# Optimization experiments

Hardware: AMD Instinct MI355X
Metric: run time of the kernel (lower is better)

Reference implementation:

```python
import jax, jax.numpy as jnp
import numpy as np

N = 40000   # nodes
E = 640000  # edges (no self loops; module adds them)
IN = 64     # in_channels
H = 8       # heads
C = 16      # hidden_channels (per head)
ED = 3      # edge_dim
OUT = 32    # last_layer_output
NEG_SLOPE = 0.2  # GATv2Conv default negative_slope


def setup_inputs() -> dict:
    key = jax.random.key(0)
    ks = jax.random.split(key, 16)
    x = jax.random.normal(ks[0], (N, IN), jnp.float32)
    src = jax.random.randint(ks[1], (E,), 0, N)
    off = jax.random.randint(ks[2], (E,), 1, N)
    dst = (src + off) % N  # guarantees no pre-existing self loops (PyG removes them anyway)
    edge_attr = jax.random.normal(ks[3], (E, ED), jnp.float32)
    HC = H * C

    def lin(k, o, i):
        return jax.random.normal(k, (o, i), jnp.float32) * (1.0 / np.sqrt(i))

    params = dict(
        Wl1=lin(ks[4], HC, IN), bl1=jnp.zeros((HC,), jnp.float32),
        Wr1=lin(ks[5], HC, IN), br1=jnp.zeros((HC,), jnp.float32),
        We1=lin(ks[6], HC, ED),
        att1=jax.random.normal(ks[7], (H, C), jnp.float32) * 0.1,
        b1=jnp.zeros((HC,), jnp.float32),
        Wl2=lin(ks[8], HC, HC), bl2=jnp.zeros((HC,), jnp.float32),
        Wr2=lin(ks[9], HC, HC), br2=jnp.zeros((HC,), jnp.float32),
        We2=lin(ks[10], HC, ED),
        att2=jax.random.normal(ks[11], (H, C), jnp.float32) * 0.1,
        b2=jnp.zeros((HC,), jnp.float32),
        Wf=lin(ks[12], OUT, HC), bf=jnp.zeros((OUT,), jnp.float32),
    )
    return {"x": x, "edge_src": src, "edge_dst": dst, "edge_attr": edge_attr, **params}


def _add_self_loops(src, dst, eattr):
    # PyG add_self_loops with fill_value='mean': self-loop attr = mean of incoming edge attrs
    sums = jax.ops.segment_sum(eattr, dst, num_segments=N)
    cnt = jax.ops.segment_sum(jnp.ones((eattr.shape[0], 1), eattr.dtype), dst, num_segments=N)
    loop = jnp.where(cnt > 0, sums / jnp.maximum(cnt, 1.0), 0.0)
    ar = jnp.arange(N)
    return (jnp.concatenate([src, ar]), jnp.concatenate([dst, ar]),
            jnp.concatenate([eattr, loop], axis=0))


def _gatv2(x, src, dst, eattr, Wl, bl, Wr, br, We, att, bias):
    xl = (x @ Wl.T + bl).reshape(-1, H, C)  # source-side transform
    xr = (x @ Wr.T + br).reshape(-1, H, C)  # target-side transform
    e = (eattr @ We.T).reshape(-1, H, C)    # edge embedding (no bias in PyG)
    m = jax.nn.leaky_relu(xl[src] + xr[dst] + e, NEG_SLOPE)  # [E', H, C]
    alpha = jnp.einsum('ehc,hc->eh', m, att)                 # attention logits
    amax = jax.ops.segment_max(alpha, dst, num_segments=N)
    ex = jnp.exp(alpha - amax[dst])
    denom = jax.ops.segment_sum(ex, dst, num_segments=N)
    a = ex / (denom[dst] + 1e-16)                            # PyG softmax epsilon
    out = jax.ops.segment_sum(xl[src] * a[:, :, None], dst, num_segments=N)
    return out.reshape(-1, H * C) + bias                      # concat heads + layer bias


def reference(x, edge_src, edge_dst, edge_attr,
              Wl1, bl1, Wr1, br1, We1, att1, b1,
              Wl2, bl2, Wr2, br2, We2, att2, b2,
              Wf, bf):
    src, dst, ea = _add_self_loops(edge_src, edge_dst, edge_attr)
    h = jax.nn.elu(_gatv2(x, src, dst, ea, Wl1, bl1, Wr1, br1, We1, att1, b1))
    h = jax.nn.elu(_gatv2(h, src, dst, ea, Wl2, bl2, Wr2, br2, We2, att2, b2))
    return h @ Wf.T + bf
```

## Files before the change

### kernel.cpp

```cpp
#include <hip/hip_runtime.h>
#include <hip/hip_fp16.h>
#include <math.h>

#define NNODES 40000
#define NEDGES 640000
#define NETOT  (NEDGES + NNODES)
#define HC 128
#define OUTC 32
#define NBLK   ((NNODES + 255) / 256)

typedef __attribute__((ext_vector_type(8))) _Float16 v8h;
typedef __attribute__((ext_vector_type(2))) _Float16 v2h;
typedef __attribute__((ext_vector_type(4))) float    v4f;

__device__ __forceinline__ unsigned splat_h(float f)
{
    unsigned short h = __half_as_ushort(__float2half(f));
    return ((unsigned)h << 16) | h;
}
__device__ __forceinline__ float h_lo(unsigned u)
{
    return __half2float(__ushort_as_half((unsigned short)(u & 0xffff)));
}
__device__ __forceinline__ v2h h2bits(unsigned u)
{
    union { unsigned u; v2h h; } c; c.u = u; return c.h;
}

#define CB ((NEDGES + 255) / 256)
#define SX4 (NNODES * 64 / 4)
#define CONV (SX4 + 2 * 128 * 64 + 2 * 128 * 128)

__global__ void count_convert_kernel(const int* __restrict__ dst, int* __restrict__ cnt,
                                     int* __restrict__ slot,
                                     const float* __restrict__ x,
                                     const float* __restrict__ Wl1, const float* __restrict__ Wr1,
                                     const float* __restrict__ Wl2, const float* __restrict__ Wr2,
                                     __half* __restrict__ x16,
                                     __half* __restrict__ WH1, __half* __restrict__ WH2)
{
    int b = blockIdx.x;
    if (b < CB) {
        int e = b * 256 + threadIdx.x;
        if (e >= NEDGES) return;
        slot[e] = atomicAdd(&cnt[dst[e]], 1);
        return;
    }
    int i = (b - CB) * 256 + threadIdx.x;
    if (i < SX4) {
        float4 v = ((const float4*)x)[i];
        __half tmp[4] = {__float2half(v.x), __float2half(v.y),
                         __float2half(v.z), __float2half(v.w)};
        ((uint2*)x16)[i] = *(const uint2*)tmp;
        return;
    }
    int j = i - SX4;
    if (j < 128 * 64)            { WH1[j] = __float2half(Wl1[j]); return; }
    j -= 128 * 64;
    if (j < 128 * 64)            { WH1[128 * 64 + j] = __float2half(Wr1[j]); return; }
    j -= 128 * 64;
    if (j < 128 * 128)           { WH2[j] = __float2half(Wl2[j]); return; }
    j -= 128 * 128;
    if (j < 128 * 128)           { WH2[128 * 128 + j] = __float2half(Wr2[j]); return; }
}

__global__ __launch_bounds__(256) void scan1_kernel(const int* __restrict__ cnt,
                                                    int* __restrict__ offsets,
                                                    int* __restrict__ blocksum)
{
    __shared__ int s[256];
    int t = threadIdx.x;
    int n = blockIdx.x * 256 + t;
    int v = (n < NNODES) ? (cnt[n] + 1) : 0;
    s[t] = v;
    __syncthreads();
    for (int off = 1; off < 256; off <<= 1) {
        int u = (t >= off) ? s[t - off] : 0;
        __syncthreads();
        s[t] += u;
        __syncthreads();
    }
    if (n < NNODES) offsets[n] = s[t] - v;
    if (t == 255) blocksum[blockIdx.x] = s[255];
}

__global__ __launch_bounds__(256) void scan2_kernel(int* __restrict__ blocksum)
{
    __shared__ int s[256];
    int t = threadIdx.x;
    int v = (t < NBLK) ? blocksum[t] : 0;
    s[t] = v;
    __syncthreads();
    for (int off = 1; off < 256; off <<= 1) {
        int u = (t >= off) ? s[t - off] : 0;
        __syncthreads();
        s[t] += u;
        __syncthreads();
    }
    if (t < NBLK) blocksum[t] = s[t] - v;
}

__global__ __launch_bounds__(256) void scan3_kernel(int* __restrict__ offsets,
                                                    const int* __restrict__ blocksum)
{
    int n = blockIdx.x * 256 + threadIdx.x;
    if (n >= NNODES) return;
    offsets[n] += blocksum[blockIdx.x];
    if (n == 0) offsets[NNODES] = NETOT;
}

__global__ void place_kernel(const int* __restrict__ src, const int* __restrict__ dst,
                             const float* __restrict__ eattr,
                             const int* __restrict__ offsets, const int* __restrict__ slot,
                             uint4* __restrict__ csr4)
{
    int e = blockIdx.x * blockDim.x + threadIdx.x;
    if (e >= NEDGES) return;
    int d = dst[e];
    int pos = offsets[d] + slot[e];
    uint4 rec;
    rec.x = (unsigned)src[e];
    rec.y = splat_h(eattr[e * 3 + 0]);
    rec.z = splat_h(eattr[e * 3 + 1]);
    rec.w = splat_h(eattr[e * 3 + 2]);
    csr4[pos] = rec;
}

__global__ __launch_bounds__(256) void loopattr_kernel(const int* __restrict__ offsets,
                                                       uint4* __restrict__ csr4)
{
    int n = blockIdx.x * 256 + threadIdx.x;
    if (n >= NNODES) return;
    int beg = offsets[n], endr = offsets[n + 1] - 1;
    float s0 = 0.f, s1 = 0.f, s2 = 0.f;
    for (int j = beg; j < endr; j++) {
        uint4 q = csr4[j];
        s0 += h_lo(q.y); s1 += h_lo(q.z); s2 += h_lo(q.w);
    }
    int c = endr - beg;
    float inv = (c > 0) ? (1.0f / (float)c) : 0.0f;
    uint4 rec;
    rec.x = (unsigned)n;
    rec.y = splat_h(s0 * inv);
    rec.z = splat_h(s1 * inv);
    rec.w = splat_h(s2 * inv);
    csr4[endr] = rec;
}

template <int K>
__global__ __launch_bounds__(256) void transform_mfma_kernel(
    const __half* __restrict__ X16, const __half* __restrict__ WH,
    const float* __restrict__ bl, const float* __restrict__ br,
    __half* __restrict__ XLo, __half* __restrict__ XRo)
{
    int t = threadIdx.x;
    int w = t >> 6, lane = t & 63;
    int nb = blockIdx.x * 32;
    int mb = w * 64;
    int l15 = lane & 15, lg = lane >> 4;

    v4f acc[4][2];
#pragma unroll
    for (int mt = 0; mt < 4; mt++)
#pragma unroll
        for (int nt = 0; nt < 2; nt++) acc[mt][nt] = (v4f){0.f, 0.f, 0.f, 0.f};

#pragma unroll
    for (int kb = 0; kb < K; kb += 32) {
        int kf = kb + lg * 8;
        v8h bfr[2], afr[4];
#pragma unroll
        for (int nt = 0; nt < 2; nt++)
            bfr[nt] = *(const v8h*)&X16[(size_t)(nb + nt * 16 + l15) * K + kf];
#pragma unroll
        for (int mt = 0; mt < 4; mt++)
            afr[mt] = *(const v8h*)&WH[(size_t)(mb + mt * 16 + l15) * K + kf];
#pragma unroll
        for (int mt = 0; mt < 4; mt++)
#pragma unroll
            for (int nt = 0; nt < 2; nt++)
                acc[mt][nt] = __builtin_amdgcn_mfma_f32_16x16x32_f16(
                    afr[mt], bfr[nt], acc[mt][nt], 0, 0, 0);
    }

    bool isR = mb >= 128;
    const float* bias = isR ? br : bl;
    __half* Out       = isR ? XRo : XLo;
    int cb = (mb & 127);
#pragma unroll
    for (int mt = 0; mt < 4; mt++) {
        int cc = cb + mt * 16 + lg * 4;
        float b0 = bias[cc], b1 = bias[cc + 1], b2 = bias[cc + 2], b3 = bias[cc + 3];
#pragma unroll
        for (int nt = 0; nt < 2; nt++) {
            int n = nb + nt * 16 + l15;
            __half tmp[4] = {__float2half(acc[mt][nt][0] + b0),
                             __float2half(acc[mt][nt][1] + b1),
                             __float2half(acc[mt][nt][2] + b2),
                             __float2half(acc[mt][nt][3] + b3)};
            *(uint2*)&Out[(size_t)n * HC + cc] = *(const uint2*)tmp;
        }
    }
}

template <int CTRL>
__device__ __forceinline__ float dpp_swap(float x)
{
    return __int_as_float(__builtin_amdgcn_update_dpp(
        0, __float_as_int(x), CTRL, 0xF, 0xF, true));
}

template <int FUSE>
__global__ __launch_bounds__(256) void agg_kernel(
    const __half* __restrict__ XL, const __half* __restrict__ XR,
    const uint4* __restrict__ csr4, const int* __restrict__ offsets,
    const float* __restrict__ We, const float* __restrict__ att,
    const float* __restrict__ bias, __half* __restrict__ OUT,
    const float* __restrict__ Wf, const float* __restrict__ bf,
    float* __restrict__ out2)
{
    __shared__ float wf_s[FUSE ? OUTC * 132 : 1];
    __shared__ float hrow[FUSE ? 4 * HC : 1];

    int t = threadIdx.x;
    if (FUSE) {
        for (int i = t * 4; i < OUTC * HC; i += 1024) {
            float4 v = *(const float4*)&Wf[i];
            *(float4*)&wf_s[(i >> 7) * 132 + (i & 127)] = v;
        }
        __syncthreads();
    }

    int w = t >> 6;
    int n = __builtin_amdgcn_readfirstlane(blockIdx.x * 4 + w);
    int lane = t & 63;
    int c0 = lane * 2;

    const float LOG2E = 1.44269504088896340736f;
    v2h xr2 = *(const v2h*)&XR[(size_t)n * HC + c0];
    float2 atf = *(const float2*)&att[c0];
    v2h at2 = {(_Float16)(atf.x * LOG2E), (_Float16)(atf.y * LOG2E)};
    v2h we0 = {(_Float16)We[c0 * 3 + 0], (_Float16)We[c0 * 3 + 3]};
    v2h we1 = {(_Float16)We[c0 * 3 + 1], (_Float16)We[c0 * 3 + 4]};
    v2h we2 = {(_Float16)We[c0 * 3 + 2], (_Float16)We[c0 * 3 + 5]};
    const v2h vk02 = {(_Float16)0.2f, (_Float16)0.2f};

    int beg = offsets[n], end = offsets[n + 1];

    float dacc[8], a0[8], a1[8];
#pragma unroll
    for (int i = 0; i < 8; i++) { dacc[i] = 0.f; a0[i] = 0.f; a1[i] = 0.f; }

#define EDGE_STEP(q, xl2, d_, a0_, a1_)                                        \
    {                                                                          \
        v2h m2 = xl2 + xr2;                                                    \
        m2 += we0 * h2bits(q.y);                                               \
        m2 += we1 * h2bits(q.z);                                               \
        m2 += we2 * h2bits(q.w);                                               \
        v2h lk = m2 * vk02;                                                    \
        m2 = __builtin_elementwise_max(m2, lk);                                \
        float p;                                                               \
        p = __builtin_amdgcn_fdot2(m2, at2, 0.0f, false);                      \
        p += dpp_swap<0xB1>(p);                                                \
        p += dpp_swap<0x4E>(p);                                                \
        p += dpp_swap<0x141>(p);                                               \
        float ex = exp2f(p);                                                   \
        d_  += ex;                                                             \
        a0_ = fmaf(ex, (float)xl2.x, a0_);                                     \
        a1_ = fmaf(ex, (float)xl2.y, a1_);                                     \
    }

    int j = beg;
    for (; j + 7 < end; j += 8) {
        uint4 q[8];
        v2h   xl[8];
#pragma unroll
        for (int i = 0; i < 8; i++) q[i] = csr4[j + i];
#pragma unroll
        for (int i = 0; i < 8; i++) {
            int s = __builtin_amdgcn_readfirstlane((int)q[i].x);
            xl[i] = *(const v2h*)&XL[((size_t)s << 7) + c0];
        }
#pragma unroll
        for (int i = 0; i < 8; i++)
            EDGE_STEP(q[i], xl[i], dacc[i], a0[i], a1[i]);
    }
    if (j + 3 < end) {
        uint4 q[4];
        v2h   xl[4];
#pragma unroll
        for (int i = 0; i < 4; i++) q[i] = csr4[j + i];
#pragma unroll
        for (int i = 0; i < 4; i++) {
            int s = __builtin_amdgcn_readfirstlane((int)q[i].x);
            xl[i] = *(const v2h*)&XL[((size_t)s << 7) + c0];
        }
#pragma unroll
        for (int i = 0; i < 4; i++)
            EDGE_STEP(q[i], xl[i], dacc[i], a0[i], a1[i]);
        j += 4;
    }
    for (; j < end; j++) {
        uint4 q = csr4[j];
        int s = __builtin_amdgcn_readfirstlane((int)q.x);
        v2h xl = *(const v2h*)&XL[((size_t)s << 7) + c0];
        EDGE_STEP(q, xl, dacc[0], a0[0], a1[0]);
    }
#undef EDGE_STEP

    float den  = ((dacc[0] + dacc[1]) + (dacc[2] + dacc[3])) +
                 ((dacc[4] + dacc[5]) + (dacc[6] + dacc[7]));
    float acc0 = ((a0[0] + a0[1]) + (a0[2] + a0[3])) +
                 ((a0[4] + a0[5]) + (a0[6] + a0[7]));
    float acc1 = ((a1[0] + a1[1]) + (a1[2] + a1[3])) +
                 ((a1[4] + a1[5]) + (a1[6] + a1[7]));

    float inv = 1.0f / (den + 1e-16f);
    float o0 = acc0 * inv + bias[c0];
    float o1 = acc1 * inv + bias[c0 + 1];
    o0 = (o0 > 0.f) ? o0 : expm1f(o0);
    o1 = (o1 > 0.f) ? o1 : expm1f(o1);

    if (!FUSE) {
        __half2 hv = __floats2half2_rn(o0, o1);
        *(__half2*)&OUT[(size_t)n * HC + c0] = hv;
    } else {
        hrow[w * HC + c0]     = o0;
        hrow[w * HC + c0 + 1] = o1;
        int o = lane & 31, half = lane >> 5;
        const float* hr = &hrow[w * HC + half * 64];
        const float* wr = &wf_s[o * 132 + half * 64];
        float acc = 0.f;
#pragma unroll
        for (int c = 0; c < 64; c += 4) {
            float4 hv = *(const float4*)&hr[c];
            float4 wv = *(const float4*)&wr[c];
            acc = fmaf(hv.x, wv.x, acc);
            acc = fmaf(hv.y, wv.y, acc);
            acc = fmaf(hv.z, wv.z, acc);
            acc = fmaf(hv.w, wv.w, acc);
        }
        acc += __shfl_xor(acc, 32);
        if (lane < 32) out2[(size_t)n * OUTC + o] = acc + bf[o];
    }
}

extern "C" void kernel_launch(void* const* d_in, const int* in_sizes, int n_in,
                              void* d_out, int out_size, void* d_ws, size_t ws_size,
                              hipStream_t stream)
{
    const float* x     = (const float*)d_in[0];
    const int*   esrc  = (const int*)d_in[1];
    const int*   edst  = (const int*)d_in[2];
    const float* eattr = (const float*)d_in[3];
    const float* Wl1 = (const float*)d_in[4];  const float* bl1 = (const float*)d_in[5];
    const float* Wr1 = (const float*)d_in[6];  const float* br1 = (const float*)d_in[7];
    const float* We1 = (const float*)d_in[8];  const float* att1 = (const float*)d_in[9];
    const float* b1  = (const float*)d_in[10];
    const float* Wl2 = (const float*)d_in[11]; const float* bl2 = (const float*)d_in[12];
    const float* Wr2 = (const float*)d_in[13]; const float* br2 = (const float*)d_in[14];
    const float* We2 = (const float*)d_in[15]; const float* att2 = (const float*)d_in[16];
    const float* b2  = (const float*)d_in[17];
    const float* Wf  = (const float*)d_in[18]; const float* bf  = (const float*)d_in[19];

    char* ws = (char*)d_ws;
    size_t off = 0;
    auto alloc = [&](size_t bytes) -> void* {
        void* p = ws + off;
        off += (bytes + 255) & ~(size_t)255;
        return p;
    };
    int*    cnt      = (int*)alloc((size_t)NNODES * 4);
    int*    offsets  = (int*)alloc((size_t)(NNODES + 1) * 4);
    int*    slot     = (int*)alloc((size_t)NEDGES * 4);
    uint4*  csr4     = (uint4*)alloc((size_t)NETOT * 16);
    int*    blocksum = (int*)alloc((size_t)NBLK * 4);
    __half* x16      = (__half*)alloc((size_t)NNODES * 64 * 2);
    __half* WH1      = (__half*)alloc((size_t)256 * 64 * 2);
    __half* WH2      = (__half*)alloc((size_t)256 * 128 * 2);
    __half* XL       = (__half*)alloc((size_t)NNODES * HC * 2);
    __half* XR       = (__half*)alloc((size_t)NNODES * HC * 2);
    __half* H1       = (__half*)alloc((size_t)NNODES * HC * 2);

    hipMemsetAsync(cnt, 0, (size_t)NNODES * 4, stream);

    count_convert_kernel<<<CB + (CONV + 255) / 256, 256, 0, stream>>>(
        edst, cnt, slot, x, Wl1, Wr1, Wl2, Wr2, x16, WH1, WH2);
    scan1_kernel<<<NBLK, 256, 0, stream>>>(cnt, offsets, blocksum);
    scan2_kernel<<<1, 256, 0, stream>>>(blocksum);
    scan3_kernel<<<NBLK, 256, 0, stream>>>(offsets, blocksum);
    place_kernel<<<(NEDGES + 255) / 256, 256, 0, stream>>>(esrc, edst, eattr, offsets, slot, csr4);
    loopattr_kernel<<<NBLK, 256, 0, stream>>>(offsets, csr4);

    transform_mfma_kernel<64><<<NNODES / 32, 256, 0, stream>>>(x16, WH1, bl1, br1, XL, XR);
    agg_kernel<0><<<NNODES / 4, 256, 0, stream>>>(XL, XR, csr4, offsets,
                                                  We1, att1, b1, H1, nullptr, nullptr, nullptr);
    transform_mfma_kernel<128><<<NNODES / 32, 256, 0, stream>>>(H1, WH2, bl2, br2, XL, XR);
    agg_kernel<1><<<NNODES / 4, 256, 0, stream>>>(XL, XR, csr4, offsets,
                                                  We2, att2, b2, nullptr, Wf, bf, (float*)d_out);
}
```

Measured before the change: 189.3 us.

## Pack CSR edge records into 8 bytes and fuse placement with first transform

Edge records shrink from 16 to 8 bytes by packing a 16-bit source index with three half-precision edge attributes. The aggregation kernels re-splat the attributes after a scalar readfirstlane. This halves CSR traffic in placement, self-loop averaging and both aggregation passes. The edge placement kernel and the layer-1 MFMA transform now run as one launch with split block ranges, removing a launch and letting the two overlap. The 16-bit source index limits node count to 65536.

```diff
diff --git a/kernel.cpp b/kernel.cpp
--- a/kernel.cpp
+++ b/kernel.cpp
@@ -13,18 +13,17 @@
 typedef __attribute__((ext_vector_type(2))) _Float16 v2h;
 typedef __attribute__((ext_vector_type(4))) float    v4f;
 
-__device__ __forceinline__ unsigned splat_h(float f)
-{
-    unsigned short h = __half_as_ushort(__float2half(f));
-    return ((unsigned)h << 16) | h;
-}
-__device__ __forceinline__ float h_lo(unsigned u)
-{
-    return __half2float(__ushort_as_half((unsigned short)(u & 0xffff)));
-}
 __device__ __forceinline__ v2h h2bits(unsigned u)
 {
     union { unsigned u; v2h h; } c; c.u = u; return c.h;
+}
+__device__ __forceinline__ float h_at(unsigned u, int hi)
+{
+    return __half2float(__ushort_as_half((unsigned short)(hi ? (u >> 16) : (u & 0xffff))));
+}
+__device__ __forceinline__ unsigned hbits(float f)
+{
+    return (unsigned)__half_as_ushort(__float2half(f));
 }
 
 #define CB ((NEDGES + 255) / 256)
@@ -109,53 +108,15 @@
     if (n == 0) offsets[NNODES] = NETOT;
 }
 
-__global__ void place_kernel(const int* __restrict__ src, const int* __restrict__ dst,
-                             const float* __restrict__ eattr,
-                             const int* __restrict__ offsets, const int* __restrict__ slot,
-                             uint4* __restrict__ csr4)
-{
-    int e = blockIdx.x * blockDim.x + threadIdx.x;
-    if (e >= NEDGES) return;
-    int d = dst[e];
-    int pos = offsets[d] + slot[e];
-    uint4 rec;
-    rec.x = (unsigned)src[e];
-    rec.y = splat_h(eattr[e * 3 + 0]);
-    rec.z = splat_h(eattr[e * 3 + 1]);
-    rec.w = splat_h(eattr[e * 3 + 2]);
-    csr4[pos] = rec;
-}
-
-__global__ __launch_bounds__(256) void loopattr_kernel(const int* __restrict__ offsets,
-                                                       uint4* __restrict__ csr4)
-{
-    int n = blockIdx.x * 256 + threadIdx.x;
-    if (n >= NNODES) return;
-    int beg = offsets[n], endr = offsets[n + 1] - 1;
-    float s0 = 0.f, s1 = 0.f, s2 = 0.f;
-    for (int j = beg; j < endr; j++) {
-        uint4 q = csr4[j];
-        s0 += h_lo(q.y); s1 += h_lo(q.z); s2 += h_lo(q.w);
-    }
-    int c = endr - beg;
-    float inv = (c > 0) ? (1.0f / (float)c) : 0.0f;
-    uint4 rec;
-    rec.x = (unsigned)n;
-    rec.y = splat_h(s0 * inv);
-    rec.z = splat_h(s1 * inv);
-    rec.w = splat_h(s2 * inv);
-    csr4[endr] = rec;
-}
-
 template <int K>
-__global__ __launch_bounds__(256) void transform_mfma_kernel(
+__device__ __forceinline__ void transform_body(
+    int bx, int t,
     const __half* __restrict__ X16, const __half* __restrict__ WH,
     const float* __restrict__ bl, const float* __restrict__ br,
     __half* __restrict__ XLo, __half* __restrict__ XRo)
 {
-    int t = threadIdx.x;
     int w = t >> 6, lane = t & 63;
-    int nb = blockIdx.x * 32;
+    int nb = bx * 32;
     int mb = w * 64;
     int l15 = lane & 15, lg = lane >> 4;
 
@@ -203,6 +164,58 @@
     }
 }
 
+template <int K>
+__global__ __launch_bounds__(256) void transform_mfma_kernel(
+    const __half* __restrict__ X16, const __half* __restrict__ WH,
+    const float* __restrict__ bl, const float* __restrict__ br,
+    __half* __restrict__ XLo, __half* __restrict__ XRo)
+{
+    transform_body<K>(blockIdx.x, threadIdx.x, X16, WH, bl, br, XLo, XRo);
+}
+
+__global__ __launch_bounds__(256) void place_transform_kernel(
+    const int* __restrict__ src, const int* __restrict__ dst,
+    const float* __restrict__ eattr,
+    const int* __restrict__ offsets, const int* __restrict__ slot,
+    uint2* __restrict__ csr2,
+    const __half* __restrict__ X16, const __half* __restrict__ WH,
+    const float* __restrict__ bl, const float* __restrict__ br,
+    __half* __restrict__ XLo, __half* __restrict__ XRo)
+{
+    int b = blockIdx.x;
+    if (b < CB) {
+        int e = b * 256 + threadIdx.x;
+        if (e >= NEDGES) return;
+        int d = dst[e];
+        int pos = offsets[d] + slot[e];
+        uint2 rec;
+        rec.x = (unsigned)src[e] | (hbits(eattr[e * 3 + 0]) << 16);
+        rec.y = hbits(eattr[e * 3 + 1]) | (hbits(eattr[e * 3 + 2]) << 16);
+        csr2[pos] = rec;
+        return;
+    }
+    transform_body<64>(b - CB, threadIdx.x, X16, WH, bl, br, XLo, XRo);
+}
+
+__global__ __launch_bounds__(256) void loopattr_kernel(const int* __restrict__ offsets,
+                                                       uint2* __restrict__ csr2)
+{
+    int n = blockIdx.x * 256 + threadIdx.x;
+    if (n >= NNODES) return;
+    int beg = offsets[n], endr = offsets[n + 1] - 1;
+    float s0 = 0.f, s1 = 0.f, s2 = 0.f;
+    for (int j = beg; j < endr; j++) {
+        uint2 q = csr2[j];
+        s0 += h_at(q.x, 1); s1 += h_at(q.y, 0); s2 += h_at(q.y, 1);
+    }
+    int c = endr - beg;
+    float inv = (c > 0) ? (1.0f / (float)c) : 0.0f;
+    uint2 rec;
+    rec.x = (unsigned)n | (hbits(s0 * inv) << 16);
+    rec.y = hbits(s1 * inv) | (hbits(s2 * inv) << 16);
+    csr2[endr] = rec;
+}
+
 template <int CTRL>
 __device__ __forceinline__ float dpp_swap(float x)
 {
@@ -213,7 +226,7 @@
 template <int FUSE>
 __global__ __launch_bounds__(256) void agg_kernel(
     const __half* __restrict__ XL, const __half* __restrict__ XR,
-    const uint4* __restrict__ csr4, const int* __restrict__ offsets,
+    const uint2* __restrict__ csr2, const int* __restrict__ offsets,
     const float* __restrict__ We, const float* __restrict__ att,
     const float* __restrict__ bias, __half* __restrict__ OUT,
     const float* __restrict__ Wf, const float* __restrict__ bf,
@@ -251,12 +264,22 @@
 #pragma unroll
     for (int i = 0; i < 8; i++) { dacc[i] = 0.f; a0[i] = 0.f; a1[i] = 0.f; }
 
-#define EDGE_STEP(q, xl2, d_, a0_, a1_)                                        \
+#define DECODE(q, s_, e00_, e11_, e22_)                                        \
+    {                                                                          \
+        unsigned qx = (unsigned)__builtin_amdgcn_readfirstlane((int)q.x);      \
+        unsigned qy = (unsigned)__builtin_amdgcn_readfirstlane((int)q.y);      \
+        s_   = (int)(qx & 0xffffu);                                            \
+        e00_ = (qx >> 16) * 0x10001u;                                          \
+        e11_ = (qy & 0xffffu) * 0x10001u;                                      \
+        e22_ = (qy & 0xffff0000u) | (qy >> 16);                                \
+    }
+
+#define EDGE_STEP(e00, e11, e22, xl2, d_, a0_, a1_)                            \
     {                                                                          \
         v2h m2 = xl2 + xr2;                                                    \
-        m2 += we0 * h2bits(q.y);                                               \
-        m2 += we1 * h2bits(q.z);                                               \
-        m2 += we2 * h2bits(q.w);                                               \
+        m2 += we0 * h2bits(e00);                                               \
+        m2 += we1 * h2bits(e11);                                               \
+        m2 += we2 * h2bits(e22);                                               \
         v2h lk = m2 * vk02;                                                    \
         m2 = __builtin_elementwise_max(m2, lk);                                \
         float p;                                                               \
@@ -272,41 +295,47 @@
 
     int j = beg;
     for (; j + 7 < end; j += 8) {
-        uint4 q[8];
+        uint2 q[8];
         v2h   xl[8];
-#pragma unroll
-        for (int i = 0; i < 8; i++) q[i] = csr4[j + i];
+        int      s[8];
+        unsigned e00[8], e11[8], e22[8];
+#pragma unroll
+        for (int i = 0; i < 8; i++) q[i] = csr2[j + i];
 #pragma unroll
         for (int i = 0; i < 8; i++) {
-            int s = __builtin_amdgcn_readfirstlane((int)q[i].x);
-            xl[i] = *(const v2h*)&XL[((size_t)s << 7) + c0];
+            DECODE(q[i], s[i], e00[i], e11[i], e22[i]);
+            xl[i] = *(const v2h*)&XL[((size_t)s[i] << 7) + c0];
         }
 #pragma unroll
         for (int i = 0; i < 8; i++)
-            EDGE_STEP(q[i], xl[i], dacc[i], a0[i], a1[i]);
+            EDGE_STEP(e00[i], e11[i], e22[i], xl[i], dacc[i], a0[i], a1[i]);
     }
     if (j + 3 < end) {
-        uint4 q[4];
+        uint2 q[4];
         v2h   xl[4];
-#pragma unroll
-        for (int i = 0; i < 4; i++) q[i] = csr4[j + i];
+        int      s[4];
+        unsigned e00[4], e11[4], e22[4];
+#pragma unroll
+        for (int i = 0; i < 4; i++) q[i] = csr2[j + i];
 #pragma unroll
         for (int i = 0; i < 4; i++) {
-            int s = __builtin_amdgcn_readfirstlane((int)q[i].x);
-            xl[i] = *(const v2h*)&XL[((size_t)s << 7) + c0];
+            DECODE(q[i], s[i], e00[i], e11[i], e22[i]);
+            xl[i] = *(const v2h*)&XL[((size_t)s[i] << 7) + c0];
         }
 #pragma unroll
         for (int i = 0; i < 4; i++)
-            EDGE_STEP(q[i], xl[i], dacc[i], a0[i], a1[i]);
+            EDGE_STEP(e00[i], e11[i], e22[i], xl[i], dacc[i], a0[i], a1[i]);
         j += 4;
     }
     for (; j < end; j++) {
-        uint4 q = csr4[j];
-        int s = __builtin_amdgcn_readfirstlane((int)q.x);
+        uint2 q = csr2[j];
+        int s; unsigned e00, e11, e22;
+        DECODE(q, s, e00, e11, e22);
         v2h xl = *(const v2h*)&XL[((size_t)s << 7) + c0];
-        EDGE_STEP(q, xl, dacc[0], a0[0], a1[0]);
+        EDGE_STEP(e00, e11, e22, xl, dacc[0], a0[0], a1[0]);
     }
 #undef EDGE_STEP
+#undef DECODE
 
     float den  = ((dacc[0] + dacc[1]) + (dacc[2] + dacc[3])) +
                  ((dacc[4] + dacc[5]) + (dacc[6] + dacc[7]));
@@ -373,7 +402,7 @@
     int*    cnt      = (int*)alloc((size_t)NNODES * 4);
     int*    offsets  = (int*)alloc((size_t)(NNODES + 1) * 4);
     int*    slot     = (int*)alloc((size_t)NEDGES * 4);
-    uint4*  csr4     = (uint4*)alloc((size_t)NETOT * 16);
+    uint2*  csr2     = (uint2*)alloc((size_t)NETOT * 8);
     int*    blocksum = (int*)alloc((size_t)NBLK * 4);
     __half* x16      = (__half*)alloc((size_t)NNODES * 64 * 2);
     __half* WH1      = (__half*)alloc((size_t)256 * 64 * 2);
@@ -389,13 +418,15 @@
     scan1_kernel<<<NBLK, 256, 0, stream>>>(cnt, offsets, blocksum);
     scan2_kernel<<<1, 256, 0, stream>>>(blocksum);
     scan3_kernel<<<NBLK, 256, 0, stream>>>(offsets, blocksum);
-    place_kernel<<<(NEDGES + 255) / 256, 256, 0, stream>>>(esrc, edst, eattr, offsets, slot, csr4);
-    loopattr_kernel<<<NBLK, 256, 0, stream>>>(offsets, csr4);
-
-    transform_mfma_kernel<64><<<NNODES / 32, 256, 0, stream>>>(x16, WH1, bl1, br1, XL, XR);
-    agg_kernel<0><<<NNODES / 4, 256, 0, stream>>>(XL, XR, csr4, offsets,
+
+    place_transform_kernel<<<CB + NNODES / 32, 256, 0, stream>>>(
+        esrc, edst, eattr, offsets, slot, csr2,
+        x16, WH1, bl1, br1, XL, XR);
+    loopattr_kernel<<<NBLK, 256, 0, stream>>>(offsets, csr2);
+
+    agg_kernel<0><<<NNODES / 4, 256, 0, stream>>>(XL, XR, csr2, offsets,
                                                   We1, att1, b1, H1, nullptr, nullptr, nullptr);
     transform_mfma_kernel<128><<<NNODES / 32, 256, 0, stream>>>(H1, WH2, bl2, br2, XL, XR);
-    agg_kernel<1><<<NNODES / 4, 256, 0, stream>>>(XL, XR, csr4, offsets,
+    agg_kernel<1><<<NNODES / 4, 256, 0, stream>>>(XL, XR, csr2, offsets,
                                                   We2, att2, b2, nullptr, Wf, bf, (float*)d_out);
 }
```

Result: faster. 180.2 us (-4.8%).

## Process two edges per wavefront in aggregation and fuse placement with layer-1 transform

Applied to the files above, without the earlier changes.

The aggregation kernel now splits each wavefront into two halves that handle alternating edges, each lane covering 4 channels of a 64-lane half-row instead of 2 channels of a full row. Partial sums are combined across the halves with a shuffle, which halves the per-edge loop trip count and widens the XL gathers. Separately, the CSR placement kernel and the layer-1 MFMA transform are merged into one launch, saving a kernel boundary. In exchange the source index is no longer wave-uniform (readfirstlane is dropped), an odd tail edge needs masking, and the head reduction now spans only two DPP steps within a 4-lane group.

```diff
diff --git a/kernel.cpp b/kernel.cpp
--- a/kernel.cpp
+++ b/kernel.cpp
@@ -13,18 +13,18 @@
 typedef __attribute__((ext_vector_type(2))) _Float16 v2h;
 typedef __attribute__((ext_vector_type(4))) float    v4f;
 
+__device__ __forceinline__ v2h h2bits(unsigned u)
+{
+    union { unsigned u; v2h h; } c; c.u = u; return c.h;
+}
+__device__ __forceinline__ float h_lo(unsigned u)
+{
+    return __half2float(__ushort_as_half((unsigned short)(u & 0xffff)));
+}
 __device__ __forceinline__ unsigned splat_h(float f)
 {
     unsigned short h = __half_as_ushort(__float2half(f));
     return ((unsigned)h << 16) | h;
-}
-__device__ __forceinline__ float h_lo(unsigned u)
-{
-    return __half2float(__ushort_as_half((unsigned short)(u & 0xffff)));
-}
-__device__ __forceinline__ v2h h2bits(unsigned u)
-{
-    union { unsigned u; v2h h; } c; c.u = u; return c.h;
 }
 
 #define CB ((NEDGES + 255) / 256)
@@ -109,21 +109,95 @@
     if (n == 0) offsets[NNODES] = NETOT;
 }
 
-__global__ void place_kernel(const int* __restrict__ src, const int* __restrict__ dst,
-                             const float* __restrict__ eattr,
-                             const int* __restrict__ offsets, const int* __restrict__ slot,
-                             uint4* __restrict__ csr4)
-{
-    int e = blockIdx.x * blockDim.x + threadIdx.x;
-    if (e >= NEDGES) return;
-    int d = dst[e];
-    int pos = offsets[d] + slot[e];
-    uint4 rec;
-    rec.x = (unsigned)src[e];
-    rec.y = splat_h(eattr[e * 3 + 0]);
-    rec.z = splat_h(eattr[e * 3 + 1]);
-    rec.w = splat_h(eattr[e * 3 + 2]);
-    csr4[pos] = rec;
+template <int K>
+__device__ __forceinline__ void transform_body(
+    int bx, int t,
+    const __half* __restrict__ X16, const __half* __restrict__ WH,
+    const float* __restrict__ bl, const float* __restrict__ br,
+    __half* __restrict__ XLo, __half* __restrict__ XRo)
+{
+    int w = t >> 6, lane = t & 63;
+    int nb = bx * 32;
+    int mb = w * 64;
+    int l15 = lane & 15, lg = lane >> 4;
+
+    v4f acc[4][2];
+#pragma unroll
+    for (int mt = 0; mt < 4; mt++)
+#pragma unroll
+        for (int nt = 0; nt < 2; nt++) acc[mt][nt] = (v4f){0.f, 0.f, 0.f, 0.f};
+
+#pragma unroll
+    for (int kb = 0; kb < K; kb += 32) {
+        int kf = kb + lg * 8;
+        v8h bfr[2], afr[4];
+#pragma unroll
+        for (int nt = 0; nt < 2; nt++)
+            bfr[nt] = *(const v8h*)&X16[(size_t)(nb + nt * 16 + l15) * K + kf];
+#pragma unroll
+        for (int mt = 0; mt < 4; mt++)
+            afr[mt] = *(const v8h*)&WH[(size_t)(mb + mt * 16 + l15) * K + kf];
+#pragma unroll
+        for (int mt = 0; mt < 4; mt++)
+#pragma unroll
+            for (int nt = 0; nt < 2; nt++)
+                acc[mt][nt] = __builtin_amdgcn_mfma_f32_16x16x32_f16(
+                    afr[mt], bfr[nt], acc[mt][nt], 0, 0, 0);
+    }
+
+    bool isR = mb >= 128;
+    const float* bias = isR ? br : bl;
+    __half* Out       = isR ? XRo : XLo;
+    int cb = (mb & 127);
+#pragma unroll
+    for (int mt = 0; mt < 4; mt++) {
+        int cc = cb + mt * 16 + lg * 4;
+        float b0 = bias[cc], b1 = bias[cc + 1], b2 = bias[cc + 2], b3 = bias[cc + 3];
+#pragma unroll
+        for (int nt = 0; nt < 2; nt++) {
+            int n = nb + nt * 16 + l15;
+            __half tmp[4] = {__float2half(acc[mt][nt][0] + b0),
+                             __float2half(acc[mt][nt][1] + b1),
+                             __float2half(acc[mt][nt][2] + b2),
+                             __float2half(acc[mt][nt][3] + b3)};
+            *(uint2*)&Out[(size_t)n * HC + cc] = *(const uint2*)tmp;
+        }
+    }
+}
+
+template <int K>
+__global__ __launch_bounds__(256) void transform_mfma_kernel(
+    const __half* __restrict__ X16, const __half* __restrict__ WH,
+    const float* __restrict__ bl, const float* __restrict__ br,
+    __half* __restrict__ XLo, __half* __restrict__ XRo)
+{
+    transform_body<K>(blockIdx.x, threadIdx.x, X16, WH, bl, br, XLo, XRo);
+}
+
+__global__ __launch_bounds__(256) void place_transform_kernel(
+    const int* __restrict__ src, const int* __restrict__ dst,
+    const float* __restrict__ eattr,
+    const int* __restrict__ offsets, const int* __restrict__ slot,
+    uint4* __restrict__ csr4,
+    const __half* __restrict__ X16, const __half* __restrict__ WH,
+    const float* __restrict__ bl, const float* __restrict__ br,
+    __half* __restrict__ XLo, __half* __restrict__ XRo)
+{
+    int b = blockIdx.x;
+    if (b < CB) {
+        int e = b * 256 + threadIdx.x;
+        if (e >= NEDGES) return;
+        int d = dst[e];
+        int pos = offsets[d] + slot[e];
+        uint4 rec;
+        rec.x = (unsigned)src[e];
+        rec.y = splat_h(eattr[e * 3 + 0]);
+        rec.z = splat_h(eattr[e * 3 + 1]);
+        rec.w = splat_h(eattr[e * 3 + 2]);
+        csr4[pos] = rec;
+        return;
+    }
+    transform_body<64>(b - CB, threadIdx.x, X16, WH, bl, br, XLo, XRo);
 }
 
 __global__ __launch_bounds__(256) void loopattr_kernel(const int* __restrict__ offsets,
@@ -147,62 +221,6 @@
     csr4[endr] = rec;
 }
 
-template <int K>
-__global__ __launch_bounds__(256) void transform_mfma_kernel(
-    const __half* __restrict__ X16, const __half* __restrict__ WH,
-    const float* __restrict__ bl, const float* __restrict__ br,
-    __half* __restrict__ XLo, __half* __restrict__ XRo)
-{
-    int t = threadIdx.x;
-    int w = t >> 6, lane = t & 63;
-    int nb = blockIdx.x * 32;
-    int mb = w * 64;
-    int l15 = lane & 15, lg = lane >> 4;
-
-    v4f acc[4][2];
-#pragma unroll
-    for (int mt = 0; mt < 4; mt++)
-#pragma unroll
-        for (int nt = 0; nt < 2; nt++) acc[mt][nt] = (v4f){0.f, 0.f, 0.f, 0.f};
-
-#pragma unroll
-    for (int kb = 0; kb < K; kb += 32) {
-        int kf = kb + lg * 8;
-        v8h bfr[2], afr[4];
-#pragma unroll
-        for (int nt = 0; nt < 2; nt++)
-            bfr[nt] = *(const v8h*)&X16[(size_t)(nb + nt * 16 + l15) * K + kf];
-#pragma unroll
-        for (int mt = 0; mt < 4; mt++)
-            afr[mt] = *(const v8h*)&WH[(size_t)(mb + mt * 16 + l15) * K + kf];
-#pragma unroll
-        for (int mt = 0; mt < 4; mt++)
-#pragma unroll
-            for (int nt = 0; nt < 2; nt++)
-                acc[mt][nt] = __builtin_amdgcn_mfma_f32_16x16x32_f16(
-                    afr[mt], bfr[nt], acc[mt][nt], 0, 0, 0);
-    }
-
-    bool isR = mb >= 128;
-    const float* bias = isR ? br : bl;
-    __half* Out       = isR ? XRo : XLo;
-    int cb = (mb & 127);
-#pragma unroll
-    for (int mt = 0; mt < 4; mt++) {
-        int cc = cb + mt * 16 + lg * 4;
-        float b0 = bias[cc], b1 = bias[cc + 1], b2 = bias[cc + 2], b3 = bias[cc + 3];
-#pragma unroll
-        for (int nt = 0; nt < 2; nt++) {
-            int n = nb + nt * 16 + l15;
-            __half tmp[4] = {__float2half(acc[mt][nt][0] + b0),
-                             __float2half(acc[mt][nt][1] + b1),
-                             __float2half(acc[mt][nt][2] + b2),
-                             __float2half(acc[mt][nt][3] + b3)};
-            *(uint2*)&Out[(size_t)n * HC + cc] = *(const uint2*)tmp;
-        }
-    }
-}
-
 template <int CTRL>
 __device__ __forceinline__ float dpp_swap(float x)
 {
@@ -234,102 +252,126 @@
     int w = t >> 6;
     int n = __builtin_amdgcn_readfirstlane(blockIdx.x * 4 + w);
     int lane = t & 63;
-    int c0 = lane * 2;
+    int half = lane >> 5;
+    int lp   = lane & 31;
+    int c0   = lp * 4;
 
     const float LOG2E = 1.44269504088896340736f;
-    v2h xr2 = *(const v2h*)&XR[(size_t)n * HC + c0];
-    float2 atf = *(const float2*)&att[c0];
-    v2h at2 = {(_Float16)(atf.x * LOG2E), (_Float16)(atf.y * LOG2E)};
-    v2h we0 = {(_Float16)We[c0 * 3 + 0], (_Float16)We[c0 * 3 + 3]};
-    v2h we1 = {(_Float16)We[c0 * 3 + 1], (_Float16)We[c0 * 3 + 4]};
-    v2h we2 = {(_Float16)We[c0 * 3 + 2], (_Float16)We[c0 * 3 + 5]};
+    uint2 xru = *(const uint2*)&XR[(size_t)n * HC + c0];
+    v2h xr2a = h2bits(xru.x), xr2b = h2bits(xru.y);
+    v2h at2a = {(_Float16)(att[c0 + 0] * LOG2E), (_Float16)(att[c0 + 1] * LOG2E)};
+    v2h at2b = {(_Float16)(att[c0 + 2] * LOG2E), (_Float16)(att[c0 + 3] * LOG2E)};
+    int cb3 = c0 * 3;
+    v2h we0a = {(_Float16)We[cb3 + 0], (_Float16)We[cb3 + 3]};
+    v2h we1a = {(_Float16)We[cb3 + 1], (_Float16)We[cb3 + 4]};
+    v2h we2a = {(_Float16)We[cb3 + 2], (_Float16)We[cb3 + 5]};
+    v2h we0b = {(_Float16)We[cb3 + 6], (_Float16)We[cb3 + 9]};
+    v2h we1b = {(_Float16)We[cb3 + 7], (_Float16)We[cb3 + 10]};
+    v2h we2b = {(_Float16)We[cb3 + 8], (_Float16)We[cb3 + 11]};
     const v2h vk02 = {(_Float16)0.2f, (_Float16)0.2f};
 
     int beg = offsets[n], end = offsets[n + 1];
 
-    float dacc[8], a0[8], a1[8];
-#pragma unroll
-    for (int i = 0; i < 8; i++) { dacc[i] = 0.f; a0[i] = 0.f; a1[i] = 0.f; }
-
-#define EDGE_STEP(q, xl2, d_, a0_, a1_)                                        \
+    float dacc[4], a0[4], a1[4], a2[4], a3[4];
+#pragma unroll
+    for (int i = 0; i < 4; i++) { dacc[i] = 0.f; a0[i] = 0.f; a1[i] = 0.f; a2[i] = 0.f; a3[i] = 0.f; }
+
+#define PAIR_STEP(qv, xlu, d_, A0, A1, A2, A3, ZTAIL)                          \
     {                                                                          \
-        v2h m2 = xl2 + xr2;                                                    \
-        m2 += we0 * h2bits(q.y);                                               \
-        m2 += we1 * h2bits(q.z);                                               \
-        m2 += we2 * h2bits(q.w);                                               \
-        v2h lk = m2 * vk02;                                                    \
-        m2 = __builtin_elementwise_max(m2, lk);                                \
-        float p;                                                               \
-        p = __builtin_amdgcn_fdot2(m2, at2, 0.0f, false);                      \
+        v2h xla = h2bits(xlu.x), xlb = h2bits(xlu.y);                          \
+        v2h ma = xla + xr2a;                                                   \
+        v2h mb = xlb + xr2b;                                                   \
+        ma += we0a * h2bits(qv.y);  mb += we0b * h2bits(qv.y);                 \
+        ma += we1a * h2bits(qv.z);  mb += we1b * h2bits(qv.z);                 \
+        ma += we2a * h2bits(qv.w);  mb += we2b * h2bits(qv.w);                 \
+        ma = __builtin_elementwise_max(ma, ma * vk02);                         \
+        mb = __builtin_elementwise_max(mb, mb * vk02);                         \
+        float p = __builtin_amdgcn_fdot2(mb, at2b, 0.0f, false);               \
+        p = __builtin_amdgcn_fdot2(ma, at2a, p, false);                        \
         p += dpp_swap<0xB1>(p);                                                \
         p += dpp_swap<0x4E>(p);                                                \
-        p += dpp_swap<0x141>(p);                                               \
         float ex = exp2f(p);                                                   \
-        d_  += ex;                                                             \
-        a0_ = fmaf(ex, (float)xl2.x, a0_);                                     \
-        a1_ = fmaf(ex, (float)xl2.y, a1_);                                     \
+        if (ZTAIL) ex = (half == 0) ? ex : 0.f;                                \
+        d_ += ex;                                                              \
+        A0 = fmaf(ex, (float)xla.x, A0);                                       \
+        A1 = fmaf(ex, (float)xla.y, A1);                                       \
+        A2 = fmaf(ex, (float)xlb.x, A2);                                       \
+        A3 = fmaf(ex, (float)xlb.y, A3);                                       \
     }
 
     int j = beg;
     for (; j + 7 < end; j += 8) {
-        uint4 q[8];
-        v2h   xl[8];
-#pragma unroll
-        for (int i = 0; i < 8; i++) q[i] = csr4[j + i];
-#pragma unroll
-        for (int i = 0; i < 8; i++) {
-            int s = __builtin_amdgcn_readfirstlane((int)q[i].x);
-            xl[i] = *(const v2h*)&XL[((size_t)s << 7) + c0];
-        }
-#pragma unroll
-        for (int i = 0; i < 8; i++)
-            EDGE_STEP(q[i], xl[i], dacc[i], a0[i], a1[i]);
+        uint4 q[4]; uint2 xlu[4];
+#pragma unroll
+        for (int i = 0; i < 4; i++) q[i] = csr4[j + 2 * i + half];
+#pragma unroll
+        for (int i = 0; i < 4; i++)
+            xlu[i] = *(const uint2*)&XL[((size_t)q[i].x << 7) + c0];
+#pragma unroll
+        for (int i = 0; i < 4; i++)
+            PAIR_STEP(q[i], xlu[i], dacc[i], a0[i], a1[i], a2[i], a3[i], false);
     }
     if (j + 3 < end) {
-        uint4 q[4];
-        v2h   xl[4];
-#pragma unroll
-        for (int i = 0; i < 4; i++) q[i] = csr4[j + i];
-#pragma unroll
-        for (int i = 0; i < 4; i++) {
-            int s = __builtin_amdgcn_readfirstlane((int)q[i].x);
-            xl[i] = *(const v2h*)&XL[((size_t)s << 7) + c0];
-        }
-#pragma unroll
-        for (int i = 0; i < 4; i++)
-            EDGE_STEP(q[i], xl[i], dacc[i], a0[i], a1[i]);
+        uint4 q[2]; uint2 xlu[2];
+#pragma unroll
+        for (int i = 0; i < 2; i++) q[i] = csr4[j + 2 * i + half];
+#pragma unroll
+        for (int i = 0; i < 2; i++)
+            xlu[i] = *(const uint2*)&XL[((size_t)q[i].x << 7) + c0];
+#pragma unroll
+        for (int i = 0; i < 2; i++)
+            PAIR_STEP(q[i], xlu[i], dacc[i], a0[i], a1[i], a2[i], a3[i], false);
         j += 4;
     }
-    for (; j < end; j++) {
+    if (j + 1 < end) {
+        uint4 q = csr4[j + half];
+        uint2 xlu = *(const uint2*)&XL[((size_t)q.x << 7) + c0];
+        PAIR_STEP(q, xlu, dacc[0], a0[0], a1[0], a2[0], a3[0], false);
+        j += 2;
+    }
+    if (j < end) {
         uint4 q = csr4[j];
-        int s = __builtin_amdgcn_readfirstlane((int)q.x);
-        v2h xl = *(const v2h*)&XL[((size_t)s << 7) + c0];
-        EDGE_STEP(q, xl, dacc[0], a0[0], a1[0]);
-    }
-#undef EDGE_STEP
-
-    float den  = ((dacc[0] + dacc[1]) + (dacc[2] + dacc[3])) +
-                 ((dacc[4] + dacc[5]) + (dacc[6] + dacc[7]));
-    float acc0 = ((a0[0] + a0[1]) + (a0[2] + a0[3])) +
-                 ((a0[4] + a0[5]) + (a0[6] + a0[7]));
-    float acc1 = ((a1[0] + a1[1]) + (a1[2] + a1[3])) +
-                 ((a1[4] + a1[5]) + (a1[6] + a1[7]));
+        uint2 xlu = *(const uint2*)&XL[((size_t)q.x << 7) + c0];
+        PAIR_STEP(q, xlu, dacc[0], a0[0], a1[0], a2[0], a3[0], true);
+    }
+#undef PAIR_STEP
+
+    float den  = (dacc[0] + dacc[1]) + (dacc[2] + dacc[3]);
+    float s0 = (a0[0] + a0[1]) + (a0[2] + a0[3]);
+    float s1 = (a1[0] + a1[1]) + (a1[2] + a1[3]);
+    float s2 = (a2[0] + a2[1]) + (a2[2] + a2[3]);
+    float s3 = (a3[0] + a3[1]) + (a3[2] + a3[3]);
+
+    den += __shfl_xor(den, 32);
+    s0  += __shfl_xor(s0, 32);
+    s1  += __shfl_xor(s1, 32);
+    s2  += __shfl_xor(s2, 32);
+    s3  += __shfl_xor(s3, 32);
 
     float inv = 1.0f / (den + 1e-16f);
-    float o0 = acc0 * inv + bias[c0];
-    float o1 = acc1 * inv + bias[c0 + 1];
+    float o0 = s0 * inv + bias[c0 + 0];
+    float o1 = s1 * inv + bias[c0 + 1];
+    float o2 = s2 * inv + bias[c0 + 2];
+    float o3 = s3 * inv + bias[c0 + 3];
     o0 = (o0 > 0.f) ? o0 : expm1f(o0);
     o1 = (o1 > 0.f) ? o1 : expm1f(o1);
+    o2 = (o2 > 0.f) ? o2 : expm1f(o2);
+    o3 = (o3 > 0.f) ? o3 : expm1f(o3);
 
     if (!FUSE) {
-        __half2 hv = __floats2half2_rn(o0, o1);
-        *(__half2*)&OUT[(size_t)n * HC + c0] = hv;
+        if (half == 0) {
+            __half tmp[4] = {__float2half(o0), __float2half(o1),
+                             __float2half(o2), __float2half(o3)};
+            *(uint2*)&OUT[(size_t)n * HC + c0] = *(const uint2*)tmp;
+        }
     } else {
-        hrow[w * HC + c0]     = o0;
-        hrow[w * HC + c0 + 1] = o1;
-        int o = lane & 31, half = lane >> 5;
-        const float* hr = &hrow[w * HC + half * 64];
-        const float* wr = &wf_s[o * 132 + half * 64];
+        if (half == 0) {
+            float4 hv = make_float4(o0, o1, o2, o3);
+            *(float4*)&hrow[w * HC + c0] = hv;
+        }
+        int o = lane & 31, hh = lane >> 5;
+        const float* hr = &hrow[w * HC + hh * 64];
+        const float* wr = &wf_s[o * 132 + hh * 64];
         float acc = 0.f;
 #pragma unroll
         for (int c = 0; c < 64; c += 4) {
@@ -389,10 +431,12 @@
     scan1_kernel<<<NBLK, 256, 0, stream>>>(cnt, offsets, blocksum);
     scan2_kernel<<<1, 256, 0, stream>>>(blocksum);
     scan3_kernel<<<NBLK, 256, 0, stream>>>(offsets, blocksum);
-    place_kernel<<<(NEDGES + 255) / 256, 256, 0, stream>>>(esrc, edst, eattr, offsets, slot, csr4);
+
+    place_transform_kernel<<<CB + NNODES / 32, 256, 0, stream>>>(
+        esrc, edst, eattr, offsets, slot, csr4,
+        x16, WH1, bl1, br1, XL, XR);
     loopattr_kernel<<<NBLK, 256, 0, stream>>>(offsets, csr4);
 
-    transform_mfma_kernel<64><<<NNODES / 32, 256, 0, stream>>>(x16, WH1, bl1, br1, XL, XR);
     agg_kernel<0><<<NNODES / 4, 256, 0, stream>>>(XL, XR, csr4, offsets,
                                                   We1, att1, b1, H1, nullptr, nullptr, nullptr);
     transform_mfma_kernel<128><<<NNODES / 32, 256, 0, stream>>>(H1, WH2, bl2, br2, XL, XR);
```

New measurement: 191.6 us. Within noise of the previous version (+1.2%).
